# Performance work log

Hardware: AMD Instinct MI355X
Metric: run time of the kernel (lower is better)

The kernel has to match this reference:

```python
import jax, jax.numpy as jnp
import numpy as np

W_WIN = 5  # sliding rank-pooling window (init arg w)
GRAY_W = np.array([0.2989, 0.587, 0.114], dtype=np.float32)  # torchvision Grayscale


def _window_weight_matrix(T, w):
    # Wmat[t, s] = rank-pooling weight of frame s inside window starting at t.
    # Window t covers frames t..t+N-1 with N = min(w, T-t); weights 2*(j+1)-N-1.
    M = np.zeros((T, T), dtype=np.float32)
    for t in range(T):
        N = min(w, T - t)
        for j in range(N):
            M[t, t + j] = 2.0 * (j + 1) - N - 1
    return jnp.asarray(M)


def setup_inputs() -> dict:
    key = jax.random.key(0)
    x = jax.random.normal(key, (8, 3, 64, 224, 224), dtype=jnp.float32)
    return {"x": x}


def reference(x):
    B, C, T, H, W = x.shape
    Wmat = _window_weight_matrix(T, W_WIN)  # [T, T], banded (bandwidth W_WIN)
    # Weighted sum over each sliding window: re[t] = sum_s Wmat[t,s] * x[:,:,s]
    re = jnp.einsum('ts,bcshw->tbchw', Wmat, x)  # [T,B,C,H,W]
    re = jax.nn.gelu(re, approximate=False)  # torch F.gelu is exact (erf)
    # Global (over B,C,H,W) min-subtract then max-normalize, per window t
    mn = re.min(axis=(1, 2, 3, 4), keepdims=True)
    re = re - mn
    mx = re.max(axis=(1, 2, 3, 4), keepdims=True)
    denom = jnp.where(mx != 0, mx, mx + 1e-5)
    re = re / denom
    # Grayscale: ITU-R 601 weighted channel sum -> 1 channel
    gray = jnp.einsum('tbchw,c->tbhw', re, jnp.asarray(GRAY_W, re.dtype))
    out = jnp.transpose(gray, (1, 0, 2, 3))[:, None]  # [B,1,T,H,W]
    mask = jnp.zeros((B, 1, W_WIN - 1, H, W), dtype=out.dtype)
    return jnp.concatenate([mask, out], axis=2)  # [B,1,T+w-1,H,W]
```

## Files before the change

### kernel.cpp

```cpp
#include <hip/hip_runtime.h>

#define HW 50176
#define HW4 12544
#define TT 64
#define NB1 1568
#define NB3 3808
#define SUMW 0.9999f

__device__ __forceinline__ float gelu_erf(float x) {
    return 0.5f * x * (1.0f + erff(0.70710678f * x));
}
__device__ __forceinline__ float fast_rcp(float v) {
    float r; asm("v_rcp_f32 %0, %1" : "=v"(r) : "v"(v)); return r;
}
__device__ __forceinline__ float gelu_fast(float x) {
    float x2 = x * x;
    float e = exp2f(-x * fmaf(0.1029433f, x2, 2.3022078f));
    return x * fast_rcp(1.0f + e);
}
__device__ __forceinline__ unsigned encf(float f) {
    unsigned u = __float_as_uint(f);
    return (u & 0x80000000u) ? ~u : (u | 0x80000000u);
}
__device__ __forceinline__ float decf(unsigned u) {
    unsigned b = (u & 0x80000000u) ? (u ^ 0x80000000u) : ~u;
    return __uint_as_float(b);
}
__device__ __forceinline__ unsigned pk_min_f16(unsigned a, unsigned b) {
    unsigned r; asm("v_pk_min_f16 %0, %1, %2" : "=v"(r) : "v"(a), "v"(b)); return r;
}
__device__ __forceinline__ unsigned pack2(float lo, float hi) {
    auto p = __builtin_amdgcn_cvt_pkrtz(lo, hi);
    return __builtin_bit_cast(unsigned, p);
}
__device__ __forceinline__ unsigned pk2(float r) {
    return pack2(r, -r);
}

template<bool WGS>
__global__ __launch_bounds__(256, 6) void k_pass1(const float* __restrict__ x,
                                                  unsigned* __restrict__ gmm,
                                                  _Float16* __restrict__ gs) {
    __shared__ unsigned smin[TT], smax[TT];
    const int tid = threadIdx.x;
    if (tid < TT) { smin[tid] = 0xFFFFFFFFu; smax[tid] = 0u; }
    __syncthreads();

    const int gid = blockIdx.x * 256 + tid;
    const int b   = gid / HW;
    const int hw  = gid - b * HW;
    const float* xa = x + ((size_t)(b * 3 + 0) * TT) * (size_t)HW + hw;
    const float* xb = x + ((size_t)(b * 3 + 1) * TT) * (size_t)HW + hw;
    const float* xc = x + ((size_t)(b * 3 + 2) * TT) * (size_t)HW + hw;
    _Float16* gp = gs + ((size_t)b * TT) * (size_t)HW + hw;

    #define LA(f) xa[(size_t)(f) * HW]
    #define LB(f) xb[(size_t)(f) * HW]
    #define LC(f) xc[(size_t)(f) * HW]

    float a0 = LA(0), a1 = LA(1), a2 = LA(2), a3 = LA(3), a4 = LA(4), pa = LA(5), qa = LA(6);
    float b0 = LB(0), b1 = LB(1), b2 = LB(2), b3 = LB(3), b4 = LB(4), pb = LB(5), qb = LB(6);
    float c0 = LC(0), c1 = LC(1), c2 = LC(2), c3 = LC(3), c4 = LC(4), pc = LC(5), qc = LC(6);

    const int lane = tid & 63;

    #pragma unroll
    for (int seg = 0; seg < 4; ++seg) {
        unsigned acc[16];
        #pragma unroll
        for (int j = 0; j < 16; ++j) acc[j] = 0x7BFF7BFFu;

        #pragma unroll
        for (int j = 0; j < 16; ++j) {
            const int t = seg * 16 + j;
            float ra, rb, rc;
            if (t < 60) {
                ra = fmaf(4.f, a4 - a0, 2.f * (a3 - a1));
                rb = fmaf(4.f, b4 - b0, 2.f * (b3 - b1));
                rc = fmaf(4.f, c4 - c0, 2.f * (c3 - c1));
            } else if (t == 60) {
                ra = fmaf(3.f, a3 - a0, a2 - a1);
                rb = fmaf(3.f, b3 - b0, b2 - b1);
                rc = fmaf(3.f, c3 - c0, c2 - c1);
            } else if (t == 61) {
                ra = 2.f * (a2 - a0); rb = 2.f * (b2 - b0); rc = 2.f * (c2 - c0);
            } else if (t == 62) {
                ra = a1 - a0; rb = b1 - b0; rc = c1 - c0;
            } else {
                ra = rb = rc = 0.f;
            }
            acc[j] = pk_min_f16(acc[j], pk_min_f16(pk_min_f16(pk2(ra), pk2(rb)), pk2(rc)));
            if constexpr (WGS) {
                float g = fmaf(0.114f, gelu_fast(rc),
                          fmaf(0.587f, gelu_fast(rb), 0.2989f * gelu_fast(ra)));
                gp[(size_t)t * HW] = (_Float16)g;
            }
            a0 = a1; a1 = a2; a2 = a3; a3 = a4; a4 = pa; pa = qa;
            b0 = b1; b1 = b2; b2 = b3; b3 = b4; b4 = pb; pb = qb;
            c0 = c1; c1 = c2; c2 = c3; c3 = c4; c4 = pc; pc = qc;
            if (t < 57) { qa = LA(t + 7); qb = LB(t + 7); qc = LC(t + 7); }
        }

        unsigned keep = 0x7BFF7BFFu;
        #pragma unroll
        for (int j = 0; j < 16; ++j) {
            unsigned a = acc[j];
            #pragma unroll
            for (int off = 32; off; off >>= 1)
                a = pk_min_f16(a, (unsigned)__shfl_xor((int)a, off, 64));
            if (lane == j) keep = a;
        }
        if (lane < 16) {
            union { unsigned u; _Float16 h[2]; } cv; cv.u = keep;
            const float amin = (float)cv.h[0];
            const float amax = -(float)cv.h[1];
            const float g0 = gelu_erf(amin), g1 = gelu_erf(amax);
            const float gmax = fmaxf(g0, g1);
            const float XSTAR = -0.7517916f;
            float gmin;
            if (amin >= XSTAR)      gmin = g0;
            else if (amax <= XSTAR) gmin = g1;
            else                    gmin = fminf(gelu_erf(XSTAR), fminf(g0, g1));
            atomicMin(&smin[seg * 16 + lane], encf(gmin));
            atomicMax(&smax[seg * 16 + lane], encf(gmax));
        }
    }
    #undef LA
    #undef LB
    #undef LC

    __syncthreads();
    if (tid < TT)            atomicMin(&gmm[tid], smin[tid]);
    else if (tid < 2 * TT)   atomicMax(&gmm[TT + tid - TT], smax[tid - TT]);
}

__global__ __launch_bounds__(256) void k_pass3(const unsigned* __restrict__ gs,
                                               const unsigned* __restrict__ gmm,
                                               float* __restrict__ out) {
    const int bid = blockIdx.x;
    const int b   = bid / 476;
    const int r   = bid - b * 476;
    const int t   = r / 7;
    const int seg = r - t * 7;
    const int base4 = seg * 1792 + threadIdx.x;
    float4* op = (float4*)out + ((size_t)b * 68 + t) * HW4 + base4;

    if (t < 4) {
        float4 z = make_float4(0.f, 0.f, 0.f, 0.f);
        #pragma unroll
        for (int k = 0; k < 7; ++k) op[k * 256] = z;
        return;
    }
    const int tm = t - 4;
    const float mn = decf(gmm[tm]);
    const float mx = decf(gmm[TT + tm]) - mn;
    const float inv = fast_rcp((mx != 0.f) ? mx : 1e-5f);
    const float A = inv, Bv = -mn * SUMW * inv;

    const uint2* gpp = (const uint2*)gs + ((size_t)b * TT + tm) * HW4 + base4;
    #pragma unroll
    for (int k = 0; k < 7; ++k) {
        uint2 v = gpp[k * 256];
        union { unsigned u; _Float16 h[2]; } lo, hi; lo.u = v.x; hi.u = v.y;
        float4 o;
        o.x = fmaf((float)lo.h[0], A, Bv);
        o.y = fmaf((float)lo.h[1], A, Bv);
        o.z = fmaf((float)hi.h[0], A, Bv);
        o.w = fmaf((float)hi.h[1], A, Bv);
        op[k * 256] = o;
    }
}

__global__ void k_consts(const unsigned* __restrict__ gmm, float* __restrict__ ab) {
    int t = threadIdx.x;
    float mn = decf(gmm[t]);
    float mx = decf(gmm[TT + t]) - mn;
    float inv = 1.0f / ((mx != 0.0f) ? mx : 1e-5f);
    ab[t]      = inv;
    ab[TT + t] = -mn * SUMW * inv;
}

__global__ __launch_bounds__(256) void k_pass2_direct(const float* __restrict__ x,
                                                      const float* __restrict__ ab,
                                                      float* __restrict__ out) {
    __shared__ float sA[TT], sB[TT];
    const int tid = threadIdx.x;
    if (tid < TT)          sA[tid] = ab[tid];
    else if (tid < 2 * TT) sB[tid - TT] = ab[tid];
    __syncthreads();

    const int pix = blockIdx.x * 256 + tid;
    const int b  = pix / HW;
    const int hw = pix - b * HW;
    const float* x0 = x + (size_t)(b * 3) * (TT * (size_t)HW) + hw;
    const float* x1 = x0 + (size_t)TT * HW;
    const float* x2 = x1 + (size_t)TT * HW;
    float* op = out + (size_t)b * (68 * (size_t)HW) + hw;

    op[0] = 0.f; op[HW] = 0.f; op[2 * (size_t)HW] = 0.f; op[3 * (size_t)HW] = 0.f;
    op += 4 * (size_t)HW;

    float a0 = x0[0], a1 = x0[HW], a2 = x0[2*HW], a3 = x0[3*HW], a4 = x0[4*HW];
    float b0 = x1[0], b1 = x1[HW], b2 = x1[2*HW], b3 = x1[3*HW], b4 = x1[4*HW];
    float c0 = x2[0], c1 = x2[HW], c2 = x2[2*HW], c3 = x2[3*HW], c4 = x2[4*HW];

    auto emit = [&](int t, float ra, float rb, float rc) {
        float gsv = 0.2989f * gelu_erf(ra) + 0.587f * gelu_erf(rb) + 0.114f * gelu_erf(rc);
        op[(size_t)t * HW] = fmaf(gsv, sA[t], sB[t]);
    };

    for (int t = 0; t < 59; ++t) {
        emit(t, 4.f*(a4-a0) + 2.f*(a3-a1), 4.f*(b4-b0) + 2.f*(b3-b1), 4.f*(c4-c0) + 2.f*(c3-c1));
        a0=a1; a1=a2; a2=a3; a3=a4; a4 = x0[(size_t)(t+5)*HW];
        b0=b1; b1=b2; b2=b3; b3=b4; b4 = x1[(size_t)(t+5)*HW];
        c0=c1; c1=c2; c2=c3; c3=c4; c4 = x2[(size_t)(t+5)*HW];
    }
    emit(59, 4.f*(a4-a0) + 2.f*(a3-a1), 4.f*(b4-b0) + 2.f*(b3-b1), 4.f*(c4-c0) + 2.f*(c3-c1));
    a0=a1; a1=a2; a2=a3; a3=a4; b0=b1; b1=b2; b2=b3; b3=b4; c0=c1; c1=c2; c2=c3; c3=c4;
    emit(60, 3.f*(a3-a0) + (a2-a1), 3.f*(b3-b0) + (b2-b1), 3.f*(c3-c0) + (c2-c1));
    a0=a1; a1=a2; a2=a3; b0=b1; b1=b2; b2=b3; c0=c1; c1=c2; c2=c3;
    emit(61, 2.f*(a2-a0), 2.f*(b2-b0), 2.f*(c2-c0));
    a0=a1; a1=a2; b0=b1; b1=b2; c0=c1; c1=c2;
    emit(62, a1-a0, b1-b0, c1-c0);
    op[63 * (size_t)HW] = sB[63];
}

extern "C" void kernel_launch(void* const* d_in, const int* in_sizes, int n_in,
                              void* d_out, int out_size, void* d_ws, size_t ws_size,
                              hipStream_t stream) {
    const float* x = (const float*)d_in[0];
    float* out = (float*)d_out;
    unsigned* gmm = (unsigned*)d_ws;
    float* ab = (float*)d_ws + 128;
    _Float16* gs = (_Float16*)((char*)d_ws + 1024);
    const size_t need = 1024 + (size_t)8 * TT * (size_t)HW * 2;

    hipMemsetAsync(gmm, 0xFF, TT * sizeof(unsigned), stream);
    hipMemsetAsync(gmm + TT, 0x00, TT * sizeof(unsigned), stream);

    if (ws_size >= need) {
        k_pass1<true><<<NB1, 256, 0, stream>>>(x, gmm, gs);
        k_pass3<<<NB3, 256, 0, stream>>>((const unsigned*)gs, gmm, out);
    } else {
        k_pass1<false><<<NB1, 256, 0, stream>>>(x, gmm, nullptr);
        k_consts<<<1, 64, 0, stream>>>(gmm, ab);
        k_pass2_direct<<<1568, 256, 0, stream>>>(x, ab, out);
    }
}
```

Before: 134.6 us.

## Split pass1 into two time-halves with float2 spatial vectorization

Pass1 now has each thread handle two adjacent pixels via float2 loads and packed fp16 stores. The 64-frame time axis is split into two 32-frame halves run as separate kernel launches, each reloading a 4-frame halo. Grid size per launch is halved and the occupancy hint drops from 6 to 5. The aim is wider memory transactions and shorter per-thread serial chains, at the cost of extra halo reads, one more launch and higher register pressure.

```diff
diff --git a/kernel.cpp b/kernel.cpp
--- a/kernel.cpp
+++ b/kernel.cpp
@@ -33,83 +33,101 @@
     auto p = __builtin_amdgcn_cvt_pkrtz(lo, hi);
     return __builtin_bit_cast(unsigned, p);
 }
-__device__ __forceinline__ unsigned pk2(float r) {
-    return pack2(r, -r);
-}
-
-template<bool WGS>
-__global__ __launch_bounds__(256, 6) void k_pass1(const float* __restrict__ x,
+__device__ __forceinline__ unsigned pk2(float r) { return pack2(r, -r); }
+
+template<int TC, bool WGS>
+__global__ __launch_bounds__(256, 5) void k_pass1(const float* __restrict__ x,
                                                   unsigned* __restrict__ gmm,
                                                   _Float16* __restrict__ gs) {
-    __shared__ unsigned smin[TT], smax[TT];
+    __shared__ unsigned smin[32], smax[32];
     const int tid = threadIdx.x;
-    if (tid < TT) { smin[tid] = 0xFFFFFFFFu; smax[tid] = 0u; }
+    if (tid < 32) smin[tid] = 0xFFFFFFFFu;
+    else if (tid < 64) smax[tid - 32] = 0u;
     __syncthreads();
 
-    const int gid = blockIdx.x * 256 + tid;
-    const int b   = gid / HW;
-    const int hw  = gid - b * HW;
-    const float* xa = x + ((size_t)(b * 3 + 0) * TT) * (size_t)HW + hw;
-    const float* xb = x + ((size_t)(b * 3 + 1) * TT) * (size_t)HW + hw;
-    const float* xc = x + ((size_t)(b * 3 + 2) * TT) * (size_t)HW + hw;
-    _Float16* gp = gs + ((size_t)b * TT) * (size_t)HW + hw;
-
-    #define LA(f) xa[(size_t)(f) * HW]
-    #define LB(f) xb[(size_t)(f) * HW]
-    #define LC(f) xc[(size_t)(f) * HW]
-
-    float a0 = LA(0), a1 = LA(1), a2 = LA(2), a3 = LA(3), a4 = LA(4), pa = LA(5), qa = LA(6);
-    float b0 = LB(0), b1 = LB(1), b2 = LB(2), b3 = LB(3), b4 = LB(4), pb = LB(5), qb = LB(6);
-    float c0 = LC(0), c1 = LC(1), c2 = LC(2), c3 = LC(3), c4 = LC(4), pc = LC(5), qc = LC(6);
+    const int bid = blockIdx.x;
+    const int b   = bid / 98;
+    const int hwb = bid - b * 98;
+    const int t0  = TC * 32;
+    const int hw  = (hwb * 256 + tid) * 2;
+    const float* xa = x + ((size_t)(b * 3 + 0) * TT + t0) * (size_t)HW + hw;
+    const float* xb = x + ((size_t)(b * 3 + 1) * TT + t0) * (size_t)HW + hw;
+    const float* xc = x + ((size_t)(b * 3 + 2) * TT + t0) * (size_t)HW + hw;
+    _Float16* gp = gs + ((size_t)b * TT + t0) * (size_t)HW + hw;
+
+    #define LA(f) (*(const float2*)(xa + (size_t)(f) * HW))
+    #define LB(f) (*(const float2*)(xb + (size_t)(f) * HW))
+    #define LC(f) (*(const float2*)(xc + (size_t)(f) * HW))
+
+    float2 a0 = LA(0), a1 = LA(1), a2 = LA(2), a3 = LA(3), a4 = LA(4), pa = LA(5), qa = LA(6);
+    float2 b0 = LB(0), b1 = LB(1), b2 = LB(2), b3 = LB(3), b4 = LB(4), pb = LB(5), qb = LB(6);
+    float2 c0 = LC(0), c1 = LC(1), c2 = LC(2), c3 = LC(3), c4 = LC(4), pc = LC(5), qc = LC(6);
 
     const int lane = tid & 63;
+    unsigned A0,A1,A2,A3,A4,A5,A6,A7,A8,A9,A10,A11,A12,A13,A14,A15;
+    #define ACC(j) (j==0?A0:j==1?A1:j==2?A2:j==3?A3:j==4?A4:j==5?A5:j==6?A6:j==7?A7: \
+                    j==8?A8:j==9?A9:j==10?A10:j==11?A11:j==12?A12:j==13?A13:j==14?A14:A15)
 
     #pragma unroll
-    for (int seg = 0; seg < 4; ++seg) {
-        unsigned acc[16];
-        #pragma unroll
-        for (int j = 0; j < 16; ++j) acc[j] = 0x7BFF7BFFu;
+    for (int g = 0; g < 2; ++g) {
+        A0=A1=A2=A3=A4=A5=A6=A7=A8=A9=A10=A11=A12=A13=A14=A15=0x7BFF7BFFu;
 
         #pragma unroll
         for (int j = 0; j < 16; ++j) {
-            const int t = seg * 16 + j;
-            float ra, rb, rc;
+            const int t = t0 + g * 16 + j;
+            float rax, ray, rbx, rby, rcx, rcy;
             if (t < 60) {
-                ra = fmaf(4.f, a4 - a0, 2.f * (a3 - a1));
-                rb = fmaf(4.f, b4 - b0, 2.f * (b3 - b1));
-                rc = fmaf(4.f, c4 - c0, 2.f * (c3 - c1));
+                rax = fmaf(4.f, a4.x-a0.x, 2.f*(a3.x-a1.x)); ray = fmaf(4.f, a4.y-a0.y, 2.f*(a3.y-a1.y));
+                rbx = fmaf(4.f, b4.x-b0.x, 2.f*(b3.x-b1.x)); rby = fmaf(4.f, b4.y-b0.y, 2.f*(b3.y-b1.y));
+                rcx = fmaf(4.f, c4.x-c0.x, 2.f*(c3.x-c1.x)); rcy = fmaf(4.f, c4.y-c0.y, 2.f*(c3.y-c1.y));
             } else if (t == 60) {
-                ra = fmaf(3.f, a3 - a0, a2 - a1);
-                rb = fmaf(3.f, b3 - b0, b2 - b1);
-                rc = fmaf(3.f, c3 - c0, c2 - c1);
+                rax = fmaf(3.f, a3.x-a0.x, a2.x-a1.x); ray = fmaf(3.f, a3.y-a0.y, a2.y-a1.y);
+                rbx = fmaf(3.f, b3.x-b0.x, b2.x-b1.x); rby = fmaf(3.f, b3.y-b0.y, b2.y-b1.y);
+                rcx = fmaf(3.f, c3.x-c0.x, c2.x-c1.x); rcy = fmaf(3.f, c3.y-c0.y, c2.y-c1.y);
             } else if (t == 61) {
-                ra = 2.f * (a2 - a0); rb = 2.f * (b2 - b0); rc = 2.f * (c2 - c0);
+                rax = 2.f*(a2.x-a0.x); ray = 2.f*(a2.y-a0.y);
+                rbx = 2.f*(b2.x-b0.x); rby = 2.f*(b2.y-b0.y);
+                rcx = 2.f*(c2.x-c0.x); rcy = 2.f*(c2.y-c0.y);
             } else if (t == 62) {
-                ra = a1 - a0; rb = b1 - b0; rc = c1 - c0;
+                rax = a1.x-a0.x; ray = a1.y-a0.y;
+                rbx = b1.x-b0.x; rby = b1.y-b0.y;
+                rcx = c1.x-c0.x; rcy = c1.y-c0.y;
             } else {
-                ra = rb = rc = 0.f;
+                rax = ray = rbx = rby = rcx = rcy = 0.f;
             }
-            acc[j] = pk_min_f16(acc[j], pk_min_f16(pk_min_f16(pk2(ra), pk2(rb)), pk2(rc)));
+            unsigned m = pk_min_f16(
+                pk_min_f16(pk_min_f16(pk2(rax), pk2(ray)), pk_min_f16(pk2(rbx), pk2(rby))),
+                pk_min_f16(pk2(rcx), pk2(rcy)));
+            ACC(j) = pk_min_f16(ACC(j), m);
             if constexpr (WGS) {
-                float g = fmaf(0.114f, gelu_fast(rc),
-                          fmaf(0.587f, gelu_fast(rb), 0.2989f * gelu_fast(ra)));
-                gp[(size_t)t * HW] = (_Float16)g;
+                float gx = fmaf(0.114f, gelu_fast(rcx), fmaf(0.587f, gelu_fast(rbx), 0.2989f * gelu_fast(rax)));
+                float gy = fmaf(0.114f, gelu_fast(rcy), fmaf(0.587f, gelu_fast(rby), 0.2989f * gelu_fast(ray)));
+                *(unsigned*)(gp + (size_t)(g * 16 + j) * HW) = pack2(gx, gy);
             }
-            a0 = a1; a1 = a2; a2 = a3; a3 = a4; a4 = pa; pa = qa;
-            b0 = b1; b1 = b2; b2 = b3; b3 = b4; b4 = pb; pb = qb;
-            c0 = c1; c1 = c2; c2 = c3; c3 = c4; c4 = pc; pc = qc;
-            if (t < 57) { qa = LA(t + 7); qb = LB(t + 7); qc = LC(t + 7); }
+            a0=a1; a1=a2; a2=a3; a3=a4; a4=pa; pa=qa;
+            b0=b1; b1=b2; b2=b3; b3=b4; b4=pb; pb=qb;
+            c0=c1; c1=c2; c2=c3; c3=c4; c4=pc; pc=qc;
+            const int rel = g * 16 + j;
+            if ((TC == 0 && rel <= 28) || (TC == 1 && rel <= 24)) {
+                qa = LA(rel + 7); qb = LB(rel + 7); qc = LC(rel + 7);
+            }
         }
 
         unsigned keep = 0x7BFF7BFFu;
-        #pragma unroll
-        for (int j = 0; j < 16; ++j) {
-            unsigned a = acc[j];
-            #pragma unroll
-            for (int off = 32; off; off >>= 1)
-                a = pk_min_f16(a, (unsigned)__shfl_xor((int)a, off, 64));
-            if (lane == j) keep = a;
-        }
+        #define BFLY(A, J) { unsigned v = A; \
+            v = pk_min_f16(v, (unsigned)__shfl_xor((int)v, 32, 64)); \
+            v = pk_min_f16(v, (unsigned)__shfl_xor((int)v, 16, 64)); \
+            v = pk_min_f16(v, (unsigned)__shfl_xor((int)v,  8, 64)); \
+            v = pk_min_f16(v, (unsigned)__shfl_xor((int)v,  4, 64)); \
+            v = pk_min_f16(v, (unsigned)__shfl_xor((int)v,  2, 64)); \
+            v = pk_min_f16(v, (unsigned)__shfl_xor((int)v,  1, 64)); \
+            if (lane == (J)) keep = v; }
+        BFLY(A0,0)  BFLY(A1,1)  BFLY(A2,2)  BFLY(A3,3)
+        BFLY(A4,4)  BFLY(A5,5)  BFLY(A6,6)  BFLY(A7,7)
+        BFLY(A8,8)  BFLY(A9,9)  BFLY(A10,10) BFLY(A11,11)
+        BFLY(A12,12) BFLY(A13,13) BFLY(A14,14) BFLY(A15,15)
+        #undef BFLY
+
         if (lane < 16) {
             union { unsigned u; _Float16 h[2]; } cv; cv.u = keep;
             const float amin = (float)cv.h[0];
@@ -121,17 +139,18 @@
             if (amin >= XSTAR)      gmin = g0;
             else if (amax <= XSTAR) gmin = g1;
             else                    gmin = fminf(gelu_erf(XSTAR), fminf(g0, g1));
-            atomicMin(&smin[seg * 16 + lane], encf(gmin));
-            atomicMax(&smax[seg * 16 + lane], encf(gmax));
+            atomicMin(&smin[g * 16 + lane], encf(gmin));
+            atomicMax(&smax[g * 16 + lane], encf(gmax));
         }
     }
+    #undef ACC
     #undef LA
     #undef LB
     #undef LC
 
     __syncthreads();
-    if (tid < TT)            atomicMin(&gmm[tid], smin[tid]);
-    else if (tid < 2 * TT)   atomicMax(&gmm[TT + tid - TT], smax[tid - TT]);
+    if (tid < 32)            atomicMin(&gmm[t0 + tid], smin[tid]);
+    else if (tid < 64)       atomicMax(&gmm[TT + t0 + tid - 32], smax[tid - 32]);
 }
 
 __global__ __launch_bounds__(256) void k_pass3(const unsigned* __restrict__ gs,
@@ -239,10 +258,12 @@
     hipMemsetAsync(gmm + TT, 0x00, TT * sizeof(unsigned), stream);
 
     if (ws_size >= need) {
-        k_pass1<true><<<NB1, 256, 0, stream>>>(x, gmm, gs);
+        k_pass1<0, true><<<NB1 / 2, 256, 0, stream>>>(x, gmm, gs);
+        k_pass1<1, true><<<NB1 / 2, 256, 0, stream>>>(x, gmm, gs);
         k_pass3<<<NB3, 256, 0, stream>>>((const unsigned*)gs, gmm, out);
     } else {
-        k_pass1<false><<<NB1, 256, 0, stream>>>(x, gmm, nullptr);
+        k_pass1<0, false><<<NB1 / 2, 256, 0, stream>>>(x, gmm, nullptr);
+        k_pass1<1, false><<<NB1 / 2, 256, 0, stream>>>(x, gmm, nullptr);
         k_consts<<<1, 64, 0, stream>>>(gmm, ab);
         k_pass2_direct<<<1568, 256, 0, stream>>>(x, ab, out);
     }
```

Result: slower. 138.2 us (+2.7%).
